# Kernel optimization log

Measured on AMD Instinct MI355X. Metric: run time of the kernel, lower is better.

The kernel has to match this reference:

```python
import jax, jax.numpy as jnp
import numpy as np

B, LQ, LT, D = 16, 576, 512, 768
H, DH = 12, 64
TOPK = 64
GATE_INIT = -4.0
EPS = 1e-5


def _layernorm(x, g, b):
    m = jnp.mean(x, axis=-1, keepdims=True)
    v = jnp.mean(jnp.square(x - m), axis=-1, keepdims=True)
    return (x - m) * jax.lax.rsqrt(v + EPS) * g + b


def setup_inputs() -> dict:
    key = jax.random.key(0)
    ks = jax.random.split(key, 8)
    s = D ** -0.5
    return {
        "x_q": jax.random.normal(ks[0], (B, LQ, D), jnp.float32),
        "x_kv": jax.random.normal(ks[1], (B, LT, D), jnp.float32),
        "kv_attn_mask": jnp.ones((B, LT), jnp.int32),
        "wq": jax.random.normal(ks[2], (D, D), jnp.float32) * s,
        "wk": jax.random.normal(ks[3], (D, D), jnp.float32) * s,
        "wv": jax.random.normal(ks[4], (D, D), jnp.float32) * s,
        "wo": jax.random.normal(ks[5], (D, D), jnp.float32) * s,
        "ln_q_g": jnp.ones((D,), jnp.float32),
        "ln_q_b": jnp.zeros((D,), jnp.float32),
        "ln_kv_g": jnp.ones((D,), jnp.float32),
        "ln_kv_b": jnp.zeros((D,), jnp.float32),
        "head_queries": jax.random.normal(ks[6], (H, DH), jnp.float32) * DH ** -0.5,
        "resid_logit": jnp.asarray(GATE_INIT, jnp.float32),
    }


def reference(x_q, x_kv, kv_attn_mask, wq, wk, wv, wo,
              ln_q_g, ln_q_b, ln_kv_g, ln_kv_b, head_queries, resid_logit):
    scale = DH ** -0.5
    Bc, Lq, _ = x_q.shape
    Lt = x_kv.shape[1]
    xq_n = _layernorm(x_q, ln_q_g, ln_q_b)
    xkv_n = _layernorm(x_kv, ln_kv_g, ln_kv_b)
    # torch Linear: y = x @ W.T
    q = (xq_n @ wq.T).reshape(Bc, Lq, H, DH).transpose(0, 2, 1, 3)   # [B,H,Lq,DH]
    k = (xkv_n @ wk.T).reshape(Bc, Lt, H, DH).transpose(0, 2, 1, 3)  # [B,H,Lt,DH]
    v = (xkv_n @ wv.T).reshape(Bc, Lt, H, DH).transpose(0, 2, 1, 3)

    valid = (kv_attn_mask != 0)  # [B,Lt]
    neg = jnp.asarray(-jnp.inf, q.dtype)

    # head-wise gate from learned head queries attending over keys
    gate_scores = jnp.einsum('hd,bhld->bhl', head_queries, k) * scale  # [B,H,Lt]
    gate_scores = jnp.where(valid[:, None, :], gate_scores, neg)
    gate_attn = jax.nn.softmax(gate_scores, axis=-1)
    c_h = jnp.einsum('bhl,bhld->bhd', gate_attn, k)
    g_logits = jnp.einsum('bhd,hd->bh', c_h, head_queries) * scale
    g_h = jax.nn.sigmoid(g_logits)[:, :, None, None]  # [B,H,1,1]

    # top-k token routing: zero out non-selected K/V (matches torch.where -> zeros)
    if TOPK and TOPK < Lt:
        _, topk_idx = jax.lax.top_k(gate_scores, TOPK)  # [B,H,K]
        keep = jax.nn.one_hot(topk_idx, Lt, dtype=q.dtype).sum(axis=-2) > 0  # [B,H,Lt]
        k = jnp.where(keep[..., None], k, 0.0)
        v = jnp.where(keep[..., None], v, 0.0)

    attn_logits = jnp.einsum('bhqd,bhkd->bhqk', q, k) * scale  # [B,H,Lq,Lt]
    attn_logits = jnp.where(valid[:, None, None, :], attn_logits, neg)
    attn = jax.nn.softmax(attn_logits, axis=-1)
    out = jnp.einsum('bhqk,bhkd->bhqd', attn, v) * g_h
    out = out.transpose(0, 2, 1, 3).reshape(Bc, Lq, H * DH)
    out = out @ wo.T
    alpha = jax.nn.sigmoid(resid_logit)
    return x_q + alpha * out
```

## Files before the change

kernel.cpp:

```cpp
#include <hip/hip_runtime.h>
#include <math.h>

#define BB 16
#define LQ 576
#define LT 512
#define DD 768
#define HH 12
#define DH 64
#define TOPK 64

typedef __attribute__((ext_vector_type(8))) short bf16x8;
typedef __attribute__((ext_vector_type(4))) float f32x4;
typedef __attribute__((ext_vector_type(4))) unsigned short u16x4;

static constexpr size_t XQBF  = 0;
static constexpr size_t XKVBF = 3538944;
static constexpr size_t WQB   = 6684672;
static constexpr size_t WKB   = 6979584;
static constexpr size_t WVB   = 7274496;
static constexpr size_t WOB   = 7569408;
static constexpr size_t QBFo  = 7864320;
static constexpr size_t KBFo  = 11403264;
static constexpr size_t IDXo  = 17694720;
static constexpr size_t VBIA  = 17707008;
static constexpr size_t NDVo  = 17719296;
static constexpr size_t GHo   = 17719488;
static constexpr size_t KCo   = 17719680;
static constexpr size_t VCTo  = 18112896;

__device__ inline unsigned short f2bf(float f) {
  union { float f; unsigned u; } v; v.f = f;
  unsigned r = v.u + 0x7FFFu + ((v.u >> 16) & 1u);
  return (unsigned short)(r >> 16);
}
__device__ inline float bf2f(unsigned short u) {
  union { unsigned u; float f; } v; v.u = ((unsigned)u) << 16;
  return v.f;
}
__device__ inline void gload_lds16(const void* src, void* dst) {
  __builtin_amdgcn_global_load_lds((const __attribute__((address_space(1))) void*)src,
                                   (__attribute__((address_space(3))) void*)dst, 16, 0, 0);
}

__global__ __launch_bounds__(256) void ln_all(const float* __restrict__ xq,
                                              const float* __restrict__ xkv,
                                              const float* __restrict__ gq,
                                              const float* __restrict__ bq,
                                              const float* __restrict__ gkv,
                                              const float* __restrict__ bkv,
                                              unsigned short* __restrict__ yq,
                                              unsigned short* __restrict__ ykv) {
  int row = blockIdx.x;
  const float *xr, *gg, *bb;
  unsigned short* yr;
  if (row < BB * LQ) {
    xr = xq + (size_t)row * DD; gg = gq; bb = bq; yr = yq + (size_t)row * DD;
  } else {
    int r = row - BB * LQ;
    xr = xkv + (size_t)r * DD; gg = gkv; bb = bkv; yr = ykv + (size_t)r * DD;
  }
  int t = threadIdx.x;
  float v0 = xr[t], v1 = xr[t + 256], v2 = xr[t + 512];
  __shared__ float red[4];
  float s = v0 + v1 + v2;
  #pragma unroll
  for (int o = 32; o > 0; o >>= 1) s += __shfl_xor(s, o);
  if ((t & 63) == 0) red[t >> 6] = s;
  __syncthreads();
  float m = (red[0] + red[1] + red[2] + red[3]) * (1.0f / 768.0f);
  float d0 = v0 - m, d1 = v1 - m, d2 = v2 - m;
  float s2 = d0 * d0 + d1 * d1 + d2 * d2;
  #pragma unroll
  for (int o = 32; o > 0; o >>= 1) s2 += __shfl_xor(s2, o);
  __syncthreads();
  if ((t & 63) == 0) red[t >> 6] = s2;
  __syncthreads();
  float var = (red[0] + red[1] + red[2] + red[3]) * (1.0f / 768.0f);
  float rs = rsqrtf(var + 1e-5f);
  yr[t]       = f2bf(d0 * rs * gg[t]       + bb[t]);
  yr[t + 256] = f2bf(d1 * rs * gg[t + 256] + bb[t + 256]);
  yr[t + 512] = f2bf(d2 * rs * gg[t + 512] + bb[t + 512]);
}

__global__ __launch_bounds__(256) void conv4(const float* __restrict__ s0, const float* __restrict__ s1,
                                             const float* __restrict__ s2, const float* __restrict__ s3,
                                             unsigned short* d0, unsigned short* d1,
                                             unsigned short* d2, unsigned short* d3) {
  const float* s; unsigned short* d;
  switch (blockIdx.y) {
    case 0: s = s0; d = d0; break;
    case 1: s = s1; d = d1; break;
    case 2: s = s2; d = d2; break;
    default: s = s3; d = d3; break;
  }
  int i = (blockIdx.x * 256 + threadIdx.x) * 4;
  float4 v = *reinterpret_cast<const float4*>(&s[i]);
  u16x4 o = { f2bf(v.x), f2bf(v.y), f2bf(v.z), f2bf(v.w) };
  *reinterpret_cast<u16x4*>(&d[i]) = o;
}


#define GEMM_PREAMBLE()                                                        \
  const int tid = threadIdx.x;                                                 \
  const int w = tid >> 6, l = tid & 63;                                        \
  const int wr = w >> 1, wc = w & 1, lq = l & 15, g = l >> 4;                  \
  const int srow = l >> 3;                                                     \
  const int scol = ((l & 7) * 16) ^ ((srow & 7) << 4);                         \
  int aoff[4][2], boff[4][2];                                                  \
  _Pragma("unroll")                                                            \
  for (int mi = 0; mi < 4; ++mi) {                                             \
    int rowa = wr * 64 + mi * 16 + lq;                                         \
    int rowb = wc * 64 + mi * 16 + lq;                                         \
    _Pragma("unroll")                                                          \
    for (int ks = 0; ks < 2; ++ks) {                                           \
      aoff[mi][ks] = rowa * 64 + (((ks * 64 + g * 16) ^ ((rowa & 7) << 4)) >> 1); \
      boff[mi][ks] = rowb * 64 + (((ks * 64 + g * 16) ^ ((rowb & 7) << 4)) >> 1); \
    }                                                                          \
  }

#define STAGE2(BUFI, T)                                                        \
  {                                                                            \
    int k0s = (T) * 64;                                                        \
    _Pragma("unroll")                                                          \
    for (int it = 0; it < 4; ++it) {                                           \
      int rbase = it * 32 + w * 8;                                             \
      gload_lds16(Asrc + (size_t)rbase * DD + k0s, &As[BUFI][rbase * 64]);     \
      gload_lds16(Bsrc + (size_t)rbase * DD + k0s, &Bs[BUFI][rbase * 64]);     \
    }                                                                          \
  }

#define COMPUTE2(BUFI)                                                         \
  {                                                                            \
    bf16x8 a[4][2], b[4][2];                                                   \
    _Pragma("unroll")                                                          \
    for (int mi = 0; mi < 4; ++mi)                                             \
      _Pragma("unroll")                                                        \
      for (int ks = 0; ks < 2; ++ks) {                                         \
        a[mi][ks] = *reinterpret_cast<const bf16x8*>(&As[BUFI][aoff[mi][ks]]); \
        b[mi][ks] = *reinterpret_cast<const bf16x8*>(&Bs[BUFI][boff[mi][ks]]); \
      }                                                                        \
    _Pragma("unroll")                                                          \
    for (int ks = 0; ks < 2; ++ks)                                             \
      _Pragma("unroll")                                                        \
      for (int mi = 0; mi < 4; ++mi)                                           \
        _Pragma("unroll")                                                      \
        for (int ni = 0; ni < 4; ++ni)                                         \
          acc[mi][ni] = __builtin_amdgcn_mfma_f32_16x16x32_bf16(               \
              a[mi][ks], b[ni][ks], acc[mi][ni], 0, 0, 0);                     \
  }

#define GEMM_KLOOP()                                                           \
  STAGE2(0, 0);                                                                \
  STAGE2(1, 1);                                                                \
  _Pragma("unroll")                                                            \
  for (int t = 0; t < 12; ++t) {                                               \
    if (t < 11) asm volatile("s_waitcnt vmcnt(8)" ::: "memory");               \
    else        asm volatile("s_waitcnt vmcnt(0)" ::: "memory");               \
    __builtin_amdgcn_sched_barrier(0);                                         \
    __builtin_amdgcn_s_barrier();                                              \
    if ((t & 1) == 0) { COMPUTE2(0); } else { COMPUTE2(1); }                   \
    __builtin_amdgcn_s_barrier();                                              \
    __builtin_amdgcn_sched_barrier(0);                                         \
    if (t + 2 < 12) {                                                          \
      if ((t & 1) == 0) { STAGE2(0, t + 2); } else { STAGE2(1, t + 2); }       \
    }                                                                          \
  }

__global__ __launch_bounds__(256, 2) void qk_gemm(const unsigned short* __restrict__ xqb,
                                                  const unsigned short* __restrict__ wqb,
                                                  const unsigned short* __restrict__ xkvb,
                                                  const unsigned short* __restrict__ wkb,
                                                  unsigned short* __restrict__ QBF,
                                                  unsigned short* __restrict__ KBF) {
  __shared__ __align__(16) unsigned short As[2][128 * 64];
  __shared__ __align__(16) unsigned short Bs[2][128 * 64];
  GEMM_PREAMBLE();

  int p = blockIdx.x;
  int bid = (p & 7) * 102 + (p >> 3);
  const unsigned short *A, *W;
  unsigned short* dst;
  int mtile, nt;
  float scale;
  if (bid < 432) {
    A = xqb; W = wqb; mtile = bid / 6; nt = bid % 6; dst = QBF; scale = 0.125f;
  } else {
    int q = bid - 432;
    A = xkvb; W = wkb; mtile = q / 6; nt = q % 6; dst = KBF; scale = 1.0f;
  }
  const int bm = mtile * 128, bn = nt * 128;
  const unsigned short* Asrc = A + (size_t)(bm + srow) * DD + (scol >> 1);
  const unsigned short* Bsrc = W + (size_t)(bn + srow) * DD + (scol >> 1);

  f32x4 acc[4][4] = {};
  GEMM_KLOOP();

  const int m_base = bm + wr * 64, n_base = bn + wc * 64;
  #pragma unroll
  for (int mi = 0; mi < 4; ++mi)
    #pragma unroll
    for (int r = 0; r < 4; ++r) {
      int m = m_base + mi * 16 + g * 4 + r;
      #pragma unroll
      for (int ni = 0; ni < 4; ++ni) {
        int n = n_base + ni * 16 + lq;
        dst[(size_t)m * DD + n] = f2bf(acc[mi][ni][r] * scale);
      }
    }
}

__global__ __launch_bounds__(256, 2) void o_gemm(const unsigned short* __restrict__ ABF,
                                                 const unsigned short* __restrict__ wob,
                                                 float* __restrict__ out,
                                                 const float* __restrict__ resid,
                                                 const float* __restrict__ gl) {
  __shared__ __align__(16) unsigned short As[2][128 * 64];
  __shared__ __align__(16) unsigned short Bs[2][128 * 64];
  GEMM_PREAMBLE();

  int p = blockIdx.x;
  int bid = (p & 7) * 54 + (p >> 3);
  const int mtile = bid / 6, nt = bid % 6;
  const int bm = mtile * 128, bn = nt * 128;
  const unsigned short* Asrc = ABF + (size_t)(bm + srow) * DD + (scol >> 1);
  const unsigned short* Bsrc = wob + (size_t)(bn + srow) * DD + (scol >> 1);

  f32x4 acc[4][4] = {};
  GEMM_KLOOP();

  float alpha = 1.0f / (1.0f + __expf(-gl[0]));
  const int m_base = bm + wr * 64, n_base = bn + wc * 64;
  #pragma unroll
  for (int mi = 0; mi < 4; ++mi)
    #pragma unroll
    for (int r = 0; r < 4; ++r) {
      int m = m_base + mi * 16 + g * 4 + r;
      #pragma unroll
      for (int ni = 0; ni < 4; ++ni) {
        int n = n_base + ni * 16 + lq;
        out[(size_t)m * DD + n] = resid[(size_t)m * DD + n] + alpha * acc[mi][ni][r];
      }
    }
}

__global__ __launch_bounds__(512) void gate_topk(const unsigned short* __restrict__ Kbuf,
                                                 const float* __restrict__ hq,
                                                 const int* __restrict__ mask,
                                                 int* __restrict__ idxo,
                                                 float* __restrict__ vbias,
                                                 float* __restrict__ ndv,
                                                 float* __restrict__ g_h,
                                                 unsigned short* __restrict__ KC) {
  int bh = blockIdx.x, b = bh / HH, h = bh % HH;
  int l = threadIdx.x;
  __shared__ __align__(16) unsigned short Kl[512 * 64];
  __shared__ float s_sc[512];
  __shared__ float s_p[512];
  __shared__ float part[8][64];
  __shared__ float red[8];
  __shared__ int wred[8];
  const float scale = 0.125f;
  const unsigned short* kr = Kbuf + ((size_t)(b * LT + l)) * DD + h * DH;
  float sc = 0.0f;
  #pragma unroll
  for (int j = 0; j < 8; ++j) {
    bf16x8 kk = *reinterpret_cast<const bf16x8*>(kr + j * 8);
    int cj = ((j ^ (l & 7)) * 8);
    *reinterpret_cast<bf16x8*>(&Kl[l * 64 + cj]) = kk;
    #pragma unroll
    for (int e = 0; e < 8; ++e) sc += bf2f((unsigned short)kk[e]) * hq[h * DH + j * 8 + e];
  }
  sc *= scale;
  bool maskv = (mask[b * LT + l] != 0);
  if (!maskv) sc = -INFINITY;
  s_sc[l] = sc;
  __syncthreads();
  float m = sc;
  #pragma unroll
  for (int o = 32; o > 0; o >>= 1) m = fmaxf(m, __shfl_xor(m, o));
  if ((l & 63) == 0) red[l >> 6] = m;
  __syncthreads();
  m = red[0];
  #pragma unroll
  for (int w = 1; w < 8; w++) m = fmaxf(m, red[w]);
  float p = expf(sc - m);
  float ssum = p;
  #pragma unroll
  for (int o = 32; o > 0; o >>= 1) ssum += __shfl_xor(ssum, o);
  __syncthreads();
  if ((l & 63) == 0) red[l >> 6] = ssum;
  __syncthreads();
  float Z = 0.0f;
  #pragma unroll
  for (int w = 0; w < 8; w++) Z += red[w];
  p /= Z;
  s_p[l] = p;
  __syncthreads();
  {
    int d = l & 63, grp = l >> 6;
    int j = d >> 3, e = d & 7;
    float cacc = 0.0f;
    #pragma unroll 4
    for (int i = 0; i < 64; ++i) {
      int t = grp * 64 + i;
      float kv = bf2f(Kl[t * 64 + ((j ^ (t & 7)) * 8) + e]);
      cacc += s_p[t] * kv;
    }
    part[grp][d] = cacc;
  }
  __syncthreads();
  if (l < 64) {
    float c = 0.0f;
    #pragma unroll
    for (int gpi = 0; gpi < 8; ++gpi) c += part[gpi][l];
    float v = c * hq[h * DH + l];
    #pragma unroll
    for (int o = 32; o > 0; o >>= 1) v += __shfl_xor(v, o);
    if (l == 0) g_h[bh] = 1.0f / (1.0f + expf(-v * scale));
  }
  float my = s_sc[l];
  int cnt = 0;
  for (int j = 0; j < LT; j++) {
    float sj = s_sc[j];
    cnt += (sj > my || (sj == my && j < l)) ? 1 : 0;
  }
  if (cnt < TOPK) {
    idxo[bh * TOPK + cnt] = l;
    vbias[bh * TOPK + cnt] = maskv ? 0.0f : -INFINITY;
    #pragma unroll
    for (int j = 0; j < 8; ++j) {
      bf16x8 kk = *reinterpret_cast<const bf16x8*>(&Kl[l * 64 + ((j ^ (l & 7)) * 8)]);
      *reinterpret_cast<bf16x8*>(&KC[(size_t)bh * 4096 + cnt * 64 + j * 8]) = kk;
    }
  }
  int dv = (maskv && cnt >= TOPK) ? 1 : 0;
  unsigned long long bal = __ballot(dv);
  if ((l & 63) == 0) wred[l >> 6] = __popcll(bal);
  __syncthreads();
  if (l == 0) {
    int nd = 0;
    #pragma unroll
    for (int w = 0; w < 8; w++) nd += wred[w];
    ndv[bh] = (float)nd;
  }
}

__global__ __launch_bounds__(256, 2) void vc_gemm(const unsigned short* __restrict__ xkvb,
                                                  const unsigned short* __restrict__ wvb,
                                                  const int* __restrict__ idxo,
                                                  unsigned short* __restrict__ VCT) {
  __shared__ __align__(16) unsigned short Xs[2][64 * 64];
  __shared__ __align__(16) unsigned short Ws[2][64 * 64];
  __shared__ int sidx[64];
  const int bh = blockIdx.x, b = bh / HH, h = bh % HH;
  const int tid = threadIdx.x;
  const int w = tid >> 6, l = tid & 63;
  const int lq = l & 15, g = l >> 4;
  if (tid < 64) sidx[tid] = idxo[bh * TOPK + tid];
  __syncthreads();
  const int srow = l >> 3;
  const int scol = ((l & 7) * 16) ^ ((srow & 7) << 4);
  const unsigned short* xsrc0 = xkvb + ((size_t)(b * LT + sidx[w * 16 + srow])) * DD + (scol >> 1);
  const unsigned short* xsrc1 = xkvb + ((size_t)(b * LT + sidx[w * 16 + 8 + srow])) * DD + (scol >> 1);
  const unsigned short* wsrc0 = wvb + ((size_t)(h * DH + w * 16 + srow)) * DD + (scol >> 1);
  const unsigned short* wsrc1 = wvb + ((size_t)(h * DH + w * 16 + 8 + srow)) * DD + (scol >> 1);

#define VC_STAGE(BUFI, T)                                                      \
  {                                                                            \
    int k0s = (T) * 64;                                                        \
    gload_lds16(xsrc0 + k0s, &Xs[BUFI][(w * 16) * 64]);                        \
    gload_lds16(xsrc1 + k0s, &Xs[BUFI][(w * 16 + 8) * 64]);                    \
    gload_lds16(wsrc0 + k0s, &Ws[BUFI][(w * 16) * 64]);                        \
    gload_lds16(wsrc1 + k0s, &Ws[BUFI][(w * 16 + 8) * 64]);                    \
  }

  f32x4 acc[4] = {};

#define VC_COMPUTE(BUFI)                                                       \
  {                                                                            \
    _Pragma("unroll")                                                          \
    for (int ks = 0; ks < 2; ++ks) {                                           \
      int arow = w * 16 + lq;                                                  \
      int acb = (ks * 64 + g * 16) ^ ((arow & 7) << 4);                        \
      bf16x8 a = *reinterpret_cast<const bf16x8*>(&Ws[BUFI][arow * 64 + (acb >> 1)]); \
      _Pragma("unroll")                                                        \
      for (int ni = 0; ni < 4; ++ni) {                                         \
        int brow = ni * 16 + lq;                                               \
        int bcb = (ks * 64 + g * 16) ^ ((brow & 7) << 4);                      \
        bf16x8 bfr = *reinterpret_cast<const bf16x8*>(&Xs[BUFI][brow * 64 + (bcb >> 1)]); \
        acc[ni] = __builtin_amdgcn_mfma_f32_16x16x32_bf16(a, bfr, acc[ni], 0, 0, 0); \
      }                                                                        \
    }                                                                          \
  }

  VC_STAGE(0, 0);
  VC_STAGE(1, 1);
  #pragma unroll
  for (int t = 0; t < 12; ++t) {
    if (t < 11) asm volatile("s_waitcnt vmcnt(4)" ::: "memory");
    else        asm volatile("s_waitcnt vmcnt(0)" ::: "memory");
    __builtin_amdgcn_sched_barrier(0);
    __builtin_amdgcn_s_barrier();
    if ((t & 1) == 0) { VC_COMPUTE(0); } else { VC_COMPUTE(1); }
    __builtin_amdgcn_s_barrier();
    __builtin_amdgcn_sched_barrier(0);
    if (t + 2 < 12) {
      if ((t & 1) == 0) { VC_STAGE(0, t + 2); } else { VC_STAGE(1, t + 2); }
    }
  }

  #pragma unroll
  for (int ni = 0; ni < 4; ++ni)
    #pragma unroll
    for (int r = 0; r < 4; ++r) {
      int d = w * 16 + g * 4 + r;
      VCT[(size_t)bh * 4096 + d * 64 + ni * 16 + lq] = f2bf(acc[ni][r]);
    }
}

__global__ __launch_bounds__(256) void attn_topk(const unsigned short* __restrict__ Qb,
                                                 const unsigned short* __restrict__ KC,
                                                 const unsigned short* __restrict__ VCT,
                                                 const float* __restrict__ vbias,
                                                 const float* __restrict__ ndv,
                                                 const float* __restrict__ g_h,
                                                 unsigned short* __restrict__ att) {
  const int bh = blockIdx.y, b = bh / HH, h = bh % HH;
  const int q0 = blockIdx.x * 64;
  const int tid = threadIdx.x;
  const int w = tid >> 6, l = tid & 63;
  const int lq = l & 15, g = l >> 4;

  __shared__ __align__(16) unsigned short Klds[64 * 64];
  __shared__ __align__(16) unsigned short Vlds[64 * 64];
  __shared__ float svb[64];

  const int srow = l >> 3;
  const int scol = ((l & 7) * 16) ^ ((srow & 7) << 4);
  #pragma unroll
  for (int it = 0; it < 2; ++it) {
    int rbase = w * 16 + it * 8;
    gload_lds16(KC  + (size_t)bh * 4096 + (rbase + srow) * 64 + (scol >> 1), &Klds[rbase * 64]);
    gload_lds16(VCT + (size_t)bh * 4096 + (rbase + srow) * 64 + (scol >> 1), &Vlds[rbase * 64]);
  }
  if (tid < 64) svb[tid] = vbias[bh * TOPK + tid];

  bf16x8 qf0, qf1;
  {
    const unsigned short* qrow =
        Qb + ((size_t)(b * LQ + q0 + w * 16 + lq)) * DD + h * DH + g * 8;
    qf0 = *reinterpret_cast<const bf16x8*>(qrow);
    qf1 = *reinterpret_cast<const bf16x8*>(qrow + 32);
  }
  __syncthreads();

  f32x4 S[4];
  #pragma unroll
  for (int kt = 0; kt < 4; ++kt) {
    f32x4 acc = {};
    int row = kt * 16 + lq;
    int c0 = (g * 16) ^ ((row & 7) << 4);
    int c1 = (64 + g * 16) ^ ((row & 7) << 4);
    bf16x8 a0 = *reinterpret_cast<const bf16x8*>(&Klds[row * 64 + (c0 >> 1)]);
    bf16x8 a1 = *reinterpret_cast<const bf16x8*>(&Klds[row * 64 + (c1 >> 1)]);
    acc = __builtin_amdgcn_mfma_f32_16x16x32_bf16(a0, qf0, acc, 0, 0, 0);
    acc = __builtin_amdgcn_mfma_f32_16x16x32_bf16(a1, qf1, acc, 0, 0, 0);
    S[kt] = acc;
  }

  float s_v[16];
  float mx = -INFINITY;
  #pragma unroll
  for (int kt = 0; kt < 4; ++kt)
    #pragma unroll
    for (int r = 0; r < 4; ++r) {
      float s = S[kt][r] + svb[kt * 16 + g * 4 + r];
      s_v[kt * 4 + r] = s;
      mx = fmaxf(mx, s);
    }
  mx = fmaxf(mx, __shfl_xor(mx, 16));
  mx = fmaxf(mx, __shfl_xor(mx, 32));
  float nd = ndv[bh];
  float m2 = (nd > 0.0f) ? fmaxf(mx, 0.0f) : mx;

  float psum = 0.0f;
  unsigned short pb[16];
  #pragma unroll
  for (int i = 0; i < 16; ++i) {
    float p = __expf(s_v[i] - m2);
    psum += p;
    pb[i] = f2bf(p);
  }
  psum += __shfl_xor(psum, 16);
  psum += __shfl_xor(psum, 32);
  float Z = psum + nd * __expf(-m2);
  float inv = 1.0f / Z;

  bf16x8 pa0, pa1;
  #pragma unroll
  for (int j = 0; j < 8; ++j) { pa0[j] = (short)pb[j]; pa1[j] = (short)pb[8 + j]; }

  f32x4 O[4] = {};
  #pragma unroll
  for (int dt = 0; dt < 4; ++dt) {
    int r = dt * 16 + lq;
    int swz = (r & 7) << 4;
    #pragma unroll
    for (int ks = 0; ks < 2; ++ks) {
      int cl = (64 * ks + g * 8) ^ swz;
      int ch = (64 * ks + 32 + g * 8) ^ swz;
      u16x4 lo = *reinterpret_cast<const u16x4*>(&Vlds[r * 64 + (cl >> 1)]);
      u16x4 hi = *reinterpret_cast<const u16x4*>(&Vlds[r * 64 + (ch >> 1)]);
      bf16x8 vb = { (short)lo[0], (short)lo[1], (short)lo[2], (short)lo[3],
                    (short)hi[0], (short)hi[1], (short)hi[2], (short)hi[3] };
      O[dt] = __builtin_amdgcn_mfma_f32_16x16x32_bf16(ks == 0 ? pa0 : pa1, vb, O[dt], 0, 0, 0);
    }
  }

  float invl[4];
  #pragma unroll
  for (int r = 0; r < 4; ++r) invl[r] = __shfl(inv, g * 4 + r);
  float gh = g_h[bh];
  #pragma unroll
  for (int dt = 0; dt < 4; ++dt)
    #pragma unroll
    for (int r = 0; r < 4; ++r) {
      int q = q0 + w * 16 + g * 4 + r;
      att[((size_t)(b * LQ + q)) * DD + h * DH + dt * 16 + lq] =
          f2bf(O[dt][r] * invl[r] * gh);
    }
}

extern "C" void kernel_launch(void* const* d_in, const int* in_sizes, int n_in,
                              void* d_out, int out_size, void* d_ws, size_t ws_size,
                              hipStream_t stream) {
  const float* x_q      = (const float*)d_in[0];
  const float* x_kv     = (const float*)d_in[1];
  const int*   mask     = (const int*)d_in[2];
  const float* wq       = (const float*)d_in[3];
  const float* wk       = (const float*)d_in[4];
  const float* wv       = (const float*)d_in[5];
  const float* wo       = (const float*)d_in[6];
  const float* ln_q_g   = (const float*)d_in[7];
  const float* ln_q_b   = (const float*)d_in[8];
  const float* ln_kv_g  = (const float*)d_in[9];
  const float* ln_kv_b  = (const float*)d_in[10];
  const float* hq       = (const float*)d_in[11];
  const float* resid_l  = (const float*)d_in[12];
  float* out = (float*)d_out;
  float* ws  = (float*)d_ws;

  unsigned short* xqb  = (unsigned short*)(ws + XQBF);
  unsigned short* xkvb = (unsigned short*)(ws + XKVBF);
  unsigned short* wqb  = (unsigned short*)(ws + WQB);
  unsigned short* wkb  = (unsigned short*)(ws + WKB);
  unsigned short* wvb  = (unsigned short*)(ws + WVB);
  unsigned short* wob  = (unsigned short*)(ws + WOB);
  unsigned short* QBF  = (unsigned short*)(ws + QBFo);
  unsigned short* KBF  = (unsigned short*)(ws + KBFo);
  int*            IDX  = (int*)(ws + IDXo);
  unsigned short* KC   = (unsigned short*)(ws + KCo);
  unsigned short* VCT  = (unsigned short*)(ws + VCTo);
  unsigned short* ABF  = xqb;

  conv4<<<dim3(576, 4), dim3(256), 0, stream>>>(wq, wk, wv, wo, wqb, wkb, wvb, wob);

  ln_all<<<dim3(BB * LQ + BB * LT), dim3(256), 0, stream>>>(x_q, x_kv, ln_q_g, ln_q_b,
                                                            ln_kv_g, ln_kv_b, xqb, xkvb);

  qk_gemm<<<dim3(816), dim3(256), 0, stream>>>(xqb, wqb, xkvb, wkb, QBF, KBF);

  gate_topk<<<dim3(BB * HH), dim3(512), 0, stream>>>(KBF, hq, mask, IDX,
                                                     ws + VBIA, ws + NDVo, ws + GHo, KC);

  vc_gemm<<<dim3(BB * HH), dim3(256), 0, stream>>>(xkvb, wvb, IDX, VCT);

  attn_topk<<<dim3(LQ / 64, BB * HH), dim3(256), 0, stream>>>(QBF, KC, VCT,
                                                              ws + VBIA, ws + NDVo, ws + GHo, ABF);

  o_gemm<<<dim3(432), dim3(256), 0, stream>>>(ABF, wob, out, x_q, resid_l);
}
```

Baseline: 115.7 us.

## Fold head queries into Wk to compute gate scores without full K projection

Precomputes u_h = hq_h·Wk_h so gate scores come from a small GEMM of normalized x_kv against 12 projected vectors, removing the full K projection over all tokens. The gate sum is computed as softmax-weighted scores instead of going through c_h. K and V are then projected only for the top-k selected tokens, fused with the Q projection into one launch. This reorders rounding: gate scores use bf16-rounded u vectors, which could flip top-k ties or near-ties relative to the reference.

```diff
diff --git a/kernel.cpp b/kernel.cpp
--- a/kernel.cpp
+++ b/kernel.cpp
@@ -20,7 +20,8 @@
 static constexpr size_t WVB   = 7274496;
 static constexpr size_t WOB   = 7569408;
 static constexpr size_t QBFo  = 7864320;
-static constexpr size_t KBFo  = 11403264;
+static constexpr size_t UBo   = 11403264;
+static constexpr size_t GSo   = 11409408;
 static constexpr size_t IDXo  = 17694720;
 static constexpr size_t VBIA  = 17707008;
 static constexpr size_t NDVo  = 17719296;
@@ -82,10 +83,31 @@
   yr[t + 512] = f2bf(d2 * rs * gg[t + 512] + bb[t + 512]);
 }
 
-__global__ __launch_bounds__(256) void conv4(const float* __restrict__ s0, const float* __restrict__ s1,
-                                             const float* __restrict__ s2, const float* __restrict__ s3,
-                                             unsigned short* d0, unsigned short* d1,
-                                             unsigned short* d2, unsigned short* d3) {
+__global__ __launch_bounds__(256) void conv4u(const float* __restrict__ s0, const float* __restrict__ s1,
+                                              const float* __restrict__ s2, const float* __restrict__ s3,
+                                              unsigned short* d0, unsigned short* d1,
+                                              unsigned short* d2, unsigned short* d3,
+                                              const float* __restrict__ hq,
+                                              unsigned short* __restrict__ UB) {
+  int t = threadIdx.x;
+  if (blockIdx.y == 4) {
+    int h = blockIdx.x;
+    if (h >= 16) return;
+    if (h < HH) {
+      float a0 = 0.0f, a1 = 0.0f, a2 = 0.0f;
+      for (int d = 0; d < DH; ++d) {
+        float sc = hq[h * DH + d];
+        const float* wr = s1 + (size_t)(h * DH + d) * DD;
+        a0 += sc * wr[t]; a1 += sc * wr[t + 256]; a2 += sc * wr[t + 512];
+      }
+      UB[h * DD + t]       = f2bf(a0 * 0.125f);
+      UB[h * DD + t + 256] = f2bf(a1 * 0.125f);
+      UB[h * DD + t + 512] = f2bf(a2 * 0.125f);
+    } else {
+      UB[h * DD + t] = 0; UB[h * DD + t + 256] = 0; UB[h * DD + t + 512] = 0;
+    }
+    return;
+  }
   const float* s; unsigned short* d;
   switch (blockIdx.y) {
     case 0: s = s0; d = d0; break;
@@ -93,30 +115,19 @@
     case 2: s = s2; d = d2; break;
     default: s = s3; d = d3; break;
   }
-  int i = (blockIdx.x * 256 + threadIdx.x) * 4;
+  int i = (blockIdx.x * 256 + t) * 4;
   float4 v = *reinterpret_cast<const float4*>(&s[i]);
   u16x4 o = { f2bf(v.x), f2bf(v.y), f2bf(v.z), f2bf(v.w) };
   *reinterpret_cast<u16x4*>(&d[i]) = o;
 }
 
 
-#define GEMM_PREAMBLE()                                                        \
+#define COMMON_PREAMBLE()                                                      \
   const int tid = threadIdx.x;                                                 \
   const int w = tid >> 6, l = tid & 63;                                        \
-  const int wr = w >> 1, wc = w & 1, lq = l & 15, g = l >> 4;                  \
+  const int lq = l & 15, g = l >> 4;                                           \
   const int srow = l >> 3;                                                     \
-  const int scol = ((l & 7) * 16) ^ ((srow & 7) << 4);                         \
-  int aoff[4][2], boff[4][2];                                                  \
-  _Pragma("unroll")                                                            \
-  for (int mi = 0; mi < 4; ++mi) {                                             \
-    int rowa = wr * 64 + mi * 16 + lq;                                         \
-    int rowb = wc * 64 + mi * 16 + lq;                                         \
-    _Pragma("unroll")                                                          \
-    for (int ks = 0; ks < 2; ++ks) {                                           \
-      aoff[mi][ks] = rowa * 64 + (((ks * 64 + g * 16) ^ ((rowa & 7) << 4)) >> 1); \
-      boff[mi][ks] = rowb * 64 + (((ks * 64 + g * 16) ^ ((rowb & 7) << 4)) >> 1); \
-    }                                                                          \
-  }
+  const int scol = ((l & 7) * 16) ^ ((srow & 7) << 4);
 
 #define STAGE2(BUFI, T)                                                        \
   {                                                                            \
@@ -149,7 +160,18 @@
               a[mi][ks], b[ni][ks], acc[mi][ni], 0, 0, 0);                     \
   }
 
-#define GEMM_KLOOP()                                                           \
+#define GEMM_MAIN()                                                            \
+  int aoff[4][2], boff[4][2];                                                  \
+  _Pragma("unroll")                                                            \
+  for (int mi = 0; mi < 4; ++mi) {                                             \
+    int rowa = wr * 64 + mi * 16 + lq;                                         \
+    int rowb = wc * 64 + mi * 16 + lq;                                         \
+    _Pragma("unroll")                                                          \
+    for (int ks = 0; ks < 2; ++ks) {                                           \
+      aoff[mi][ks] = rowa * 64 + (((ks * 64 + g * 16) ^ ((rowa & 7) << 4)) >> 1); \
+      boff[mi][ks] = rowb * 64 + (((ks * 64 + g * 16) ^ ((rowb & 7) << 4)) >> 1); \
+    }                                                                          \
+  }                                                                            \
   STAGE2(0, 0);                                                                \
   STAGE2(1, 1);                                                                \
   _Pragma("unroll")                                                            \
@@ -166,47 +188,241 @@
     }                                                                          \
   }
 
-__global__ __launch_bounds__(256, 2) void qk_gemm(const unsigned short* __restrict__ xqb,
-                                                  const unsigned short* __restrict__ wqb,
-                                                  const unsigned short* __restrict__ xkvb,
-                                                  const unsigned short* __restrict__ wkb,
-                                                  unsigned short* __restrict__ QBF,
-                                                  unsigned short* __restrict__ KBF) {
+__global__ __launch_bounds__(256) void gs_gemm(const unsigned short* __restrict__ xkvb,
+                                               const unsigned short* __restrict__ UB,
+                                               float* __restrict__ GS) {
+  __shared__ __align__(16) unsigned short Xs[2][64 * 64];
+  __shared__ __align__(16) unsigned short Us[2][16 * 64];
+  COMMON_PREAMBLE();
+  const int bm = blockIdx.x * 64;
+  const unsigned short* Asrc = xkvb + (size_t)(bm + srow) * DD + (scol >> 1);
+  const unsigned short* Us0 = UB + (size_t)srow * DD + (scol >> 1);
+  const unsigned short* Us1 = UB + (size_t)(8 + srow) * DD + (scol >> 1);
+
+#define GS_STAGE(BUFI, T)                                                      \
+  {                                                                            \
+    int k0s = (T) * 64;                                                        \
+    _Pragma("unroll")                                                          \
+    for (int it = 0; it < 2; ++it) {                                           \
+      int rbase = it * 32 + w * 8;                                             \
+      gload_lds16(Asrc + (size_t)rbase * DD + k0s, &Xs[BUFI][rbase * 64]);     \
+    }                                                                          \
+    gload_lds16(Us0 + k0s, &Us[BUFI][0]);                                      \
+    gload_lds16(Us1 + k0s, &Us[BUFI][8 * 64]);                                 \
+  }
+
+  f32x4 acc = {};
+
+#define GS_COMPUTE(BUFI)                                                       \
+  {                                                                            \
+    _Pragma("unroll")                                                          \
+    for (int ks = 0; ks < 2; ++ks) {                                           \
+      int arow = w * 16 + lq;                                                  \
+      int acb = (ks * 64 + g * 16) ^ ((arow & 7) << 4);                        \
+      bf16x8 a = *reinterpret_cast<const bf16x8*>(&Xs[BUFI][arow * 64 + (acb >> 1)]); \
+      int brow = lq;                                                           \
+      int bcb = (ks * 64 + g * 16) ^ ((brow & 7) << 4);                        \
+      bf16x8 b = *reinterpret_cast<const bf16x8*>(&Us[BUFI][brow * 64 + (bcb >> 1)]); \
+      acc = __builtin_amdgcn_mfma_f32_16x16x32_bf16(a, b, acc, 0, 0, 0);       \
+    }                                                                          \
+  }
+
+  GS_STAGE(0, 0);
+  GS_STAGE(1, 1);
+  #pragma unroll
+  for (int t = 0; t < 12; ++t) {
+    if (t < 11) asm volatile("s_waitcnt vmcnt(4)" ::: "memory");
+    else        asm volatile("s_waitcnt vmcnt(0)" ::: "memory");
+    __builtin_amdgcn_sched_barrier(0);
+    __builtin_amdgcn_s_barrier();
+    if ((t & 1) == 0) { GS_COMPUTE(0); } else { GS_COMPUTE(1); }
+    __builtin_amdgcn_s_barrier();
+    __builtin_amdgcn_sched_barrier(0);
+    if (t + 2 < 12) {
+      if ((t & 1) == 0) { GS_STAGE(0, t + 2); } else { GS_STAGE(1, t + 2); }
+    }
+  }
+  #pragma unroll
+  for (int r = 0; r < 4; ++r)
+    GS[(size_t)(bm + w * 16 + g * 4 + r) * 16 + lq] = acc[r];
+}
+
+__global__ __launch_bounds__(512) void gate_topk(const float* __restrict__ GS,
+                                                 const int* __restrict__ mask,
+                                                 int* __restrict__ idxo,
+                                                 float* __restrict__ vbias,
+                                                 float* __restrict__ ndv,
+                                                 float* __restrict__ g_h) {
+  int bh = blockIdx.x, b = bh / HH, h = bh % HH;
+  int l = threadIdx.x;
+  __shared__ float s_sc[512];
+  __shared__ float red[8];
+  __shared__ int wred[8];
+  float sc = GS[(size_t)(b * LT + l) * 16 + h];
+  bool maskv = (mask[b * LT + l] != 0);
+  if (!maskv) sc = -INFINITY;
+  s_sc[l] = sc;
+  float m0 = sc;
+  #pragma unroll
+  for (int o = 32; o > 0; o >>= 1) m0 = fmaxf(m0, __shfl_xor(m0, o));
+  if ((l & 63) == 0) red[l >> 6] = m0;
+  __syncthreads();
+  float m = red[0];
+  #pragma unroll
+  for (int w = 1; w < 8; w++) m = fmaxf(m, red[w]);
+  float p = __expf(sc - m);
+  float s1 = p;
+  #pragma unroll
+  for (int o = 32; o > 0; o >>= 1) s1 += __shfl_xor(s1, o);
+  __syncthreads();
+  if ((l & 63) == 0) red[l >> 6] = s1;
+  __syncthreads();
+  float Z = 0.0f;
+  #pragma unroll
+  for (int w = 0; w < 8; w++) Z += red[w];
+  p /= Z;
+  float gc = maskv ? p * sc : 0.0f;
+  #pragma unroll
+  for (int o = 32; o > 0; o >>= 1) gc += __shfl_xor(gc, o);
+  __syncthreads();
+  if ((l & 63) == 0) red[l >> 6] = gc;
+  __syncthreads();
+  if (l == 0) {
+    float G = 0.0f;
+    #pragma unroll
+    for (int w = 0; w < 8; w++) G += red[w];
+    g_h[bh] = 1.0f / (1.0f + __expf(-G));
+  }
+  float my = s_sc[l];
+  int cnt = 0;
+  for (int j = 0; j < LT; j++) {
+    float sj = s_sc[j];
+    cnt += (sj > my || (sj == my && j < l)) ? 1 : 0;
+  }
+  if (cnt < TOPK) {
+    idxo[bh * TOPK + cnt] = l;
+    vbias[bh * TOPK + cnt] = maskv ? 0.0f : -INFINITY;
+  }
+  int dv = (maskv && cnt >= TOPK) ? 1 : 0;
+  unsigned long long bal = __ballot(dv);
+  if ((l & 63) == 0) wred[l >> 6] = __popcll(bal);
+  __syncthreads();
+  if (l == 0) {
+    int nd = 0;
+    #pragma unroll
+    for (int w = 0; w < 8; w++) nd += wred[w];
+    ndv[bh] = (float)nd;
+  }
+}
+
+__global__ __launch_bounds__(256, 2) void proj2(const unsigned short* __restrict__ xqb,
+                                                const unsigned short* __restrict__ wqb,
+                                                const unsigned short* __restrict__ xkvb,
+                                                const unsigned short* __restrict__ wkb,
+                                                const unsigned short* __restrict__ wvb,
+                                                const int* __restrict__ idxo,
+                                                unsigned short* __restrict__ QBF,
+                                                unsigned short* __restrict__ KC,
+                                                unsigned short* __restrict__ VCT) {
   __shared__ __align__(16) unsigned short As[2][128 * 64];
   __shared__ __align__(16) unsigned short Bs[2][128 * 64];
-  GEMM_PREAMBLE();
-
+  __shared__ int sidx[64];
+  COMMON_PREAMBLE();
   int p = blockIdx.x;
-  int bid = (p & 7) * 102 + (p >> 3);
-  const unsigned short *A, *W;
-  unsigned short* dst;
-  int mtile, nt;
-  float scale;
+  int bid = (p & 7) * 78 + (p >> 3);
+
   if (bid < 432) {
-    A = xqb; W = wqb; mtile = bid / 6; nt = bid % 6; dst = QBF; scale = 0.125f;
+    const int wr = w >> 1, wc = w & 1;
+    const int mtile = bid / 6, nt = bid % 6;
+    const int bm = mtile * 128, bn = nt * 128;
+    const unsigned short* Asrc = xqb + (size_t)(bm + srow) * DD + (scol >> 1);
+    const unsigned short* Bsrc = wqb + (size_t)(bn + srow) * DD + (scol >> 1);
+    f32x4 acc[4][4] = {};
+    GEMM_MAIN();
+    const int m_base = bm + wr * 64, n_base = bn + wc * 64;
+    #pragma unroll
+    for (int mi = 0; mi < 4; ++mi)
+      #pragma unroll
+      for (int r = 0; r < 4; ++r) {
+        int m = m_base + mi * 16 + g * 4 + r;
+        #pragma unroll
+        for (int ni = 0; ni < 4; ++ni) {
+          int n = n_base + ni * 16 + lq;
+          QBF[(size_t)m * DD + n] = f2bf(acc[mi][ni][r] * 0.125f);
+        }
+      }
   } else {
-    int q = bid - 432;
-    A = xkvb; W = wkb; mtile = q / 6; nt = q % 6; dst = KBF; scale = 1.0f;
-  }
-  const int bm = mtile * 128, bn = nt * 128;
-  const unsigned short* Asrc = A + (size_t)(bm + srow) * DD + (scol >> 1);
-  const unsigned short* Bsrc = W + (size_t)(bn + srow) * DD + (scol >> 1);
-
-  f32x4 acc[4][4] = {};
-  GEMM_KLOOP();
-
-  const int m_base = bm + wr * 64, n_base = bn + wc * 64;
-  #pragma unroll
-  for (int mi = 0; mi < 4; ++mi)
-    #pragma unroll
-    for (int r = 0; r < 4; ++r) {
-      int m = m_base + mi * 16 + g * 4 + r;
+    const int bh = bid - 432, b = bh / HH, h = bh % HH;
+    if (tid < 64) sidx[tid] = idxo[bh * TOPK + tid];
+    __syncthreads();
+    unsigned short* Xs0 = &As[0][0]; unsigned short* Xs1 = &As[0][4096];
+    unsigned short* Kp0 = &As[1][0]; unsigned short* Kp1 = &As[1][4096];
+    unsigned short* Vp0 = &Bs[0][0]; unsigned short* Vp1 = &Bs[0][4096];
+    const int j0 = w * 16 + srow, j1 = w * 16 + 8 + srow;
+    const unsigned short* xs0 = xkvb + (size_t)(b * LT + sidx[j0]) * DD + (scol >> 1);
+    const unsigned short* xs1 = xkvb + (size_t)(b * LT + sidx[j1]) * DD + (scol >> 1);
+    const unsigned short* wk0 = wkb + (size_t)(h * DH + j0) * DD + (scol >> 1);
+    const unsigned short* wk1 = wkb + (size_t)(h * DH + j1) * DD + (scol >> 1);
+    const unsigned short* wv0 = wvb + (size_t)(h * DH + j0) * DD + (scol >> 1);
+    const unsigned short* wv1 = wvb + (size_t)(h * DH + j1) * DD + (scol >> 1);
+
+#define KV_STAGE(Xd, Kd, Vd, T)                                                \
+    {                                                                          \
+      int k0s = (T) * 64;                                                      \
+      gload_lds16(xs0 + k0s, Xd + (w * 16) * 64);                              \
+      gload_lds16(xs1 + k0s, Xd + (w * 16 + 8) * 64);                          \
+      gload_lds16(wk0 + k0s, Kd + (w * 16) * 64);                              \
+      gload_lds16(wk1 + k0s, Kd + (w * 16 + 8) * 64);                          \
+      gload_lds16(wv0 + k0s, Vd + (w * 16) * 64);                              \
+      gload_lds16(wv1 + k0s, Vd + (w * 16 + 8) * 64);                          \
+    }
+
+    f32x4 accK[4] = {}, accV[4] = {};
+
+#define KV_COMPUTE(Xd, Kd, Vd)                                                 \
+    {                                                                          \
+      _Pragma("unroll")                                                        \
+      for (int ks = 0; ks < 2; ++ks) {                                         \
+        int arow = w * 16 + lq;                                                \
+        int acb = (ks * 64 + g * 16) ^ ((arow & 7) << 4);                      \
+        bf16x8 ax = *reinterpret_cast<const bf16x8*>(&Xd[arow * 64 + (acb >> 1)]); \
+        bf16x8 av = *reinterpret_cast<const bf16x8*>(&Vd[arow * 64 + (acb >> 1)]); \
+        _Pragma("unroll")                                                      \
+        for (int ni = 0; ni < 4; ++ni) {                                       \
+          int brow = ni * 16 + lq;                                             \
+          int bcb = (ks * 64 + g * 16) ^ ((brow & 7) << 4);                    \
+          bf16x8 bk = *reinterpret_cast<const bf16x8*>(&Kd[brow * 64 + (bcb >> 1)]); \
+          accK[ni] = __builtin_amdgcn_mfma_f32_16x16x32_bf16(ax, bk, accK[ni], 0, 0, 0); \
+          bf16x8 bx = *reinterpret_cast<const bf16x8*>(&Xd[brow * 64 + (bcb >> 1)]); \
+          accV[ni] = __builtin_amdgcn_mfma_f32_16x16x32_bf16(av, bx, accV[ni], 0, 0, 0); \
+        }                                                                      \
+      }                                                                        \
+    }
+
+    KV_STAGE(Xs0, Kp0, Vp0, 0);
+    KV_STAGE(Xs1, Kp1, Vp1, 1);
+    #pragma unroll
+    for (int t = 0; t < 12; ++t) {
+      if (t < 11) asm volatile("s_waitcnt vmcnt(6)" ::: "memory");
+      else        asm volatile("s_waitcnt vmcnt(0)" ::: "memory");
+      __builtin_amdgcn_sched_barrier(0);
+      __builtin_amdgcn_s_barrier();
+      if ((t & 1) == 0) { KV_COMPUTE(Xs0, Kp0, Vp0); } else { KV_COMPUTE(Xs1, Kp1, Vp1); }
+      __builtin_amdgcn_s_barrier();
+      __builtin_amdgcn_sched_barrier(0);
+      if (t + 2 < 12) {
+        if ((t & 1) == 0) { KV_STAGE(Xs0, Kp0, Vp0, t + 2); } else { KV_STAGE(Xs1, Kp1, Vp1, t + 2); }
+      }
+    }
+    #pragma unroll
+    for (int ni = 0; ni < 4; ++ni)
       #pragma unroll
-      for (int ni = 0; ni < 4; ++ni) {
-        int n = n_base + ni * 16 + lq;
-        dst[(size_t)m * DD + n] = f2bf(acc[mi][ni][r] * scale);
+      for (int r = 0; r < 4; ++r) {
+        int mrow = w * 16 + g * 4 + r;
+        KC [(size_t)bh * 4096 + mrow * 64 + ni * 16 + lq] = f2bf(accK[ni][r]);
+        VCT[(size_t)bh * 4096 + mrow * 64 + ni * 16 + lq] = f2bf(accV[ni][r]);
       }
-    }
+  }
 }
 
 __global__ __launch_bounds__(256, 2) void o_gemm(const unsigned short* __restrict__ ABF,
@@ -216,8 +432,8 @@
                                                  const float* __restrict__ gl) {
   __shared__ __align__(16) unsigned short As[2][128 * 64];
   __shared__ __align__(16) unsigned short Bs[2][128 * 64];
-  GEMM_PREAMBLE();
-
+  COMMON_PREAMBLE();
+  const int wr = w >> 1, wc = w & 1;
   int p = blockIdx.x;
   int bid = (p & 7) * 54 + (p >> 3);
   const int mtile = bid / 6, nt = bid % 6;
@@ -226,7 +442,7 @@
   const unsigned short* Bsrc = wob + (size_t)(bn + srow) * DD + (scol >> 1);
 
   f32x4 acc[4][4] = {};
-  GEMM_KLOOP();
+  GEMM_MAIN();
 
   float alpha = 1.0f / (1.0f + __expf(-gl[0]));
   const int m_base = bm + wr * 64, n_base = bn + wc * 64;
@@ -240,181 +456,6 @@
         int n = n_base + ni * 16 + lq;
         out[(size_t)m * DD + n] = resid[(size_t)m * DD + n] + alpha * acc[mi][ni][r];
       }
-    }
-}
-
-__global__ __launch_bounds__(512) void gate_topk(const unsigned short* __restrict__ Kbuf,
-                                                 const float* __restrict__ hq,
-                                                 const int* __restrict__ mask,
-                                                 int* __restrict__ idxo,
-                                                 float* __restrict__ vbias,
-                                                 float* __restrict__ ndv,
-                                                 float* __restrict__ g_h,
-                                                 unsigned short* __restrict__ KC) {
-  int bh = blockIdx.x, b = bh / HH, h = bh % HH;
-  int l = threadIdx.x;
-  __shared__ __align__(16) unsigned short Kl[512 * 64];
-  __shared__ float s_sc[512];
-  __shared__ float s_p[512];
-  __shared__ float part[8][64];
-  __shared__ float red[8];
-  __shared__ int wred[8];
-  const float scale = 0.125f;
-  const unsigned short* kr = Kbuf + ((size_t)(b * LT + l)) * DD + h * DH;
-  float sc = 0.0f;
-  #pragma unroll
-  for (int j = 0; j < 8; ++j) {
-    bf16x8 kk = *reinterpret_cast<const bf16x8*>(kr + j * 8);
-    int cj = ((j ^ (l & 7)) * 8);
-    *reinterpret_cast<bf16x8*>(&Kl[l * 64 + cj]) = kk;
-    #pragma unroll
-    for (int e = 0; e < 8; ++e) sc += bf2f((unsigned short)kk[e]) * hq[h * DH + j * 8 + e];
-  }
-  sc *= scale;
-  bool maskv = (mask[b * LT + l] != 0);
-  if (!maskv) sc = -INFINITY;
-  s_sc[l] = sc;
-  __syncthreads();
-  float m = sc;
-  #pragma unroll
-  for (int o = 32; o > 0; o >>= 1) m = fmaxf(m, __shfl_xor(m, o));
-  if ((l & 63) == 0) red[l >> 6] = m;
-  __syncthreads();
-  m = red[0];
-  #pragma unroll
-  for (int w = 1; w < 8; w++) m = fmaxf(m, red[w]);
-  float p = expf(sc - m);
-  float ssum = p;
-  #pragma unroll
-  for (int o = 32; o > 0; o >>= 1) ssum += __shfl_xor(ssum, o);
-  __syncthreads();
-  if ((l & 63) == 0) red[l >> 6] = ssum;
-  __syncthreads();
-  float Z = 0.0f;
-  #pragma unroll
-  for (int w = 0; w < 8; w++) Z += red[w];
-  p /= Z;
-  s_p[l] = p;
-  __syncthreads();
-  {
-    int d = l & 63, grp = l >> 6;
-    int j = d >> 3, e = d & 7;
-    float cacc = 0.0f;
-    #pragma unroll 4
-    for (int i = 0; i < 64; ++i) {
-      int t = grp * 64 + i;
-      float kv = bf2f(Kl[t * 64 + ((j ^ (t & 7)) * 8) + e]);
-      cacc += s_p[t] * kv;
-    }
-    part[grp][d] = cacc;
-  }
-  __syncthreads();
-  if (l < 64) {
-    float c = 0.0f;
-    #pragma unroll
-    for (int gpi = 0; gpi < 8; ++gpi) c += part[gpi][l];
-    float v = c * hq[h * DH + l];
-    #pragma unroll
-    for (int o = 32; o > 0; o >>= 1) v += __shfl_xor(v, o);
-    if (l == 0) g_h[bh] = 1.0f / (1.0f + expf(-v * scale));
-  }
-  float my = s_sc[l];
-  int cnt = 0;
-  for (int j = 0; j < LT; j++) {
-    float sj = s_sc[j];
-    cnt += (sj > my || (sj == my && j < l)) ? 1 : 0;
-  }
-  if (cnt < TOPK) {
-    idxo[bh * TOPK + cnt] = l;
-    vbias[bh * TOPK + cnt] = maskv ? 0.0f : -INFINITY;
-    #pragma unroll
-    for (int j = 0; j < 8; ++j) {
-      bf16x8 kk = *reinterpret_cast<const bf16x8*>(&Kl[l * 64 + ((j ^ (l & 7)) * 8)]);
-      *reinterpret_cast<bf16x8*>(&KC[(size_t)bh * 4096 + cnt * 64 + j * 8]) = kk;
-    }
-  }
-  int dv = (maskv && cnt >= TOPK) ? 1 : 0;
-  unsigned long long bal = __ballot(dv);
-  if ((l & 63) == 0) wred[l >> 6] = __popcll(bal);
-  __syncthreads();
-  if (l == 0) {
-    int nd = 0;
-    #pragma unroll
-    for (int w = 0; w < 8; w++) nd += wred[w];
-    ndv[bh] = (float)nd;
-  }
-}
-
-__global__ __launch_bounds__(256, 2) void vc_gemm(const unsigned short* __restrict__ xkvb,
-                                                  const unsigned short* __restrict__ wvb,
-                                                  const int* __restrict__ idxo,
-                                                  unsigned short* __restrict__ VCT) {
-  __shared__ __align__(16) unsigned short Xs[2][64 * 64];
-  __shared__ __align__(16) unsigned short Ws[2][64 * 64];
-  __shared__ int sidx[64];
-  const int bh = blockIdx.x, b = bh / HH, h = bh % HH;
-  const int tid = threadIdx.x;
-  const int w = tid >> 6, l = tid & 63;
-  const int lq = l & 15, g = l >> 4;
-  if (tid < 64) sidx[tid] = idxo[bh * TOPK + tid];
-  __syncthreads();
-  const int srow = l >> 3;
-  const int scol = ((l & 7) * 16) ^ ((srow & 7) << 4);
-  const unsigned short* xsrc0 = xkvb + ((size_t)(b * LT + sidx[w * 16 + srow])) * DD + (scol >> 1);
-  const unsigned short* xsrc1 = xkvb + ((size_t)(b * LT + sidx[w * 16 + 8 + srow])) * DD + (scol >> 1);
-  const unsigned short* wsrc0 = wvb + ((size_t)(h * DH + w * 16 + srow)) * DD + (scol >> 1);
-  const unsigned short* wsrc1 = wvb + ((size_t)(h * DH + w * 16 + 8 + srow)) * DD + (scol >> 1);
-
-#define VC_STAGE(BUFI, T)                                                      \
-  {                                                                            \
-    int k0s = (T) * 64;                                                        \
-    gload_lds16(xsrc0 + k0s, &Xs[BUFI][(w * 16) * 64]);                        \
-    gload_lds16(xsrc1 + k0s, &Xs[BUFI][(w * 16 + 8) * 64]);                    \
-    gload_lds16(wsrc0 + k0s, &Ws[BUFI][(w * 16) * 64]);                        \
-    gload_lds16(wsrc1 + k0s, &Ws[BUFI][(w * 16 + 8) * 64]);                    \
-  }
-
-  f32x4 acc[4] = {};
-
-#define VC_COMPUTE(BUFI)                                                       \
-  {                                                                            \
-    _Pragma("unroll")                                                          \
-    for (int ks = 0; ks < 2; ++ks) {                                           \
-      int arow = w * 16 + lq;                                                  \
-      int acb = (ks * 64 + g * 16) ^ ((arow & 7) << 4);                        \
-      bf16x8 a = *reinterpret_cast<const bf16x8*>(&Ws[BUFI][arow * 64 + (acb >> 1)]); \
-      _Pragma("unroll")                                                        \
-      for (int ni = 0; ni < 4; ++ni) {                                         \
-        int brow = ni * 16 + lq;                                               \
-        int bcb = (ks * 64 + g * 16) ^ ((brow & 7) << 4);                      \
-        bf16x8 bfr = *reinterpret_cast<const bf16x8*>(&Xs[BUFI][brow * 64 + (bcb >> 1)]); \
-        acc[ni] = __builtin_amdgcn_mfma_f32_16x16x32_bf16(a, bfr, acc[ni], 0, 0, 0); \
-      }                                                                        \
-    }                                                                          \
-  }
-
-  VC_STAGE(0, 0);
-  VC_STAGE(1, 1);
-  #pragma unroll
-  for (int t = 0; t < 12; ++t) {
-    if (t < 11) asm volatile("s_waitcnt vmcnt(4)" ::: "memory");
-    else        asm volatile("s_waitcnt vmcnt(0)" ::: "memory");
-    __builtin_amdgcn_sched_barrier(0);
-    __builtin_amdgcn_s_barrier();
-    if ((t & 1) == 0) { VC_COMPUTE(0); } else { VC_COMPUTE(1); }
-    __builtin_amdgcn_s_barrier();
-    __builtin_amdgcn_sched_barrier(0);
-    if (t + 2 < 12) {
-      if ((t & 1) == 0) { VC_STAGE(0, t + 2); } else { VC_STAGE(1, t + 2); }
-    }
-  }
-
-  #pragma unroll
-  for (int ni = 0; ni < 4; ++ni)
-    #pragma unroll
-    for (int r = 0; r < 4; ++r) {
-      int d = w * 16 + g * 4 + r;
-      VCT[(size_t)bh * 4096 + d * 64 + ni * 16 + lq] = f2bf(acc[ni][r]);
     }
 }
 
@@ -557,23 +598,24 @@
   unsigned short* wvb  = (unsigned short*)(ws + WVB);
   unsigned short* wob  = (unsigned short*)(ws + WOB);
   unsigned short* QBF  = (unsigned short*)(ws + QBFo);
-  unsigned short* KBF  = (unsigned short*)(ws + KBFo);
+  unsigned short* UB   = (unsigned short*)(ws + UBo);
+  float*          GS   = (float*)(ws + GSo);
   int*            IDX  = (int*)(ws + IDXo);
   unsigned short* KC   = (unsigned short*)(ws + KCo);
   unsigned short* VCT  = (unsigned short*)(ws + VCTo);
   unsigned short* ABF  = xqb;
 
-  conv4<<<dim3(576, 4), dim3(256), 0, stream>>>(wq, wk, wv, wo, wqb, wkb, wvb, wob);
+  conv4u<<<dim3(576, 5), dim3(256), 0, stream>>>(wq, wk, wv, wo, wqb, wkb, wvb, wob, hq, UB);
 
   ln_all<<<dim3(BB * LQ + BB * LT), dim3(256), 0, stream>>>(x_q, x_kv, ln_q_g, ln_q_b,
                                                             ln_kv_g, ln_kv_b, xqb, xkvb);
 
-  qk_gemm<<<dim3(816), dim3(256), 0, stream>>>(xqb, wqb, xkvb, wkb, QBF, KBF);
-
-  gate_topk<<<dim3(BB * HH), dim3(512), 0, stream>>>(KBF, hq, mask, IDX,
-                                                     ws + VBIA, ws + NDVo, ws + GHo, KC);
-
-  vc_gemm<<<dim3(BB * HH), dim3(256), 0, stream>>>(xkvb, wvb, IDX, VCT);
+  gs_gemm<<<dim3(128), dim3(256), 0, stream>>>(xkvb, UB, GS);
+
+  gate_topk<<<dim3(BB * HH), dim3(512), 0, stream>>>(GS, mask, IDX,
+                                                     ws + VBIA, ws + NDVo, ws + GHo);
+
+  proj2<<<dim3(624), dim3(256), 0, stream>>>(xqb, wqb, xkvb, wkb, wvb, IDX, QBF, KC, VCT);
 
   attn_topk<<<dim3(LQ / 64, BB * HH), dim3(256), 0, stream>>>(QBF, KC, VCT,
                                                               ws + VBIA, ws + NDVo, ws + GHo, ABF);
```

After: 110.5 us. 4.5% less time.
